# Optimization experiments

Hardware: AMD Instinct MI355X
Metric: run time of the kernel (lower is better)

## Reference

```python
import jax, jax.numpy as jnp
import numpy as np

D_MODEL = 768
N_HEADS = 12
N_KV = 4
D_HEAD = 64
WINDOW = 512
GLOBAL = 64
THETA = 10000.0


def setup_inputs() -> dict:
    key = jax.random.key(0)
    ks = jax.random.split(key, 5)
    B, T = 2, 2048
    s = D_MODEL ** -0.5
    return {
        "x": jax.random.normal(ks[0], (B, T, D_MODEL), jnp.float32),
        "wq": jax.random.normal(ks[1], (D_MODEL, N_HEADS * D_HEAD), jnp.float32) * s,
        "wk": jax.random.normal(ks[2], (D_MODEL, N_KV * D_HEAD), jnp.float32) * s,
        "wv": jax.random.normal(ks[3], (D_MODEL, N_KV * D_HEAD), jnp.float32) * s,
        "wo": jax.random.normal(ks[4], (N_HEADS * D_HEAD, D_MODEL), jnp.float32) * s,
    }


def _rotate_half(x):
    h = x.shape[-1] // 2
    return jnp.concatenate([-x[..., h:], x[..., :h]], axis=-1)


def _rope_tables(T, dtype):
    inv_freq = 1.0 / (THETA ** (jnp.arange(0, D_HEAD, 2, dtype=jnp.float32) / D_HEAD))
    freqs = jnp.outer(jnp.arange(T, dtype=jnp.float32), inv_freq)  # [T, D_HEAD/2]
    emb = jnp.concatenate([freqs, freqs], axis=-1)  # [T, D_HEAD]
    return jnp.cos(emb).astype(dtype), jnp.sin(emb).astype(dtype)


def reference(x, wq, wk, wv, wo):
    B, T, _ = x.shape
    # projections -> [B, H, T, D]
    q = (x @ wq).reshape(B, T, N_HEADS, D_HEAD).transpose(0, 2, 1, 3)
    k = (x @ wk).reshape(B, T, N_KV, D_HEAD).transpose(0, 2, 1, 3)
    v = (x @ wv).reshape(B, T, N_KV, D_HEAD).transpose(0, 2, 1, 3)
    # RoPE (broadcast [T,D] over batch/heads)
    cos, sin = _rope_tables(T, x.dtype)
    q = q * cos + _rotate_half(q) * sin
    k = k * cos + _rotate_half(k) * sin
    new_k, new_v = k, v  # kv cache before GQA expansion
    # GQA expansion: each kv head repeated kv_groups consecutive times
    groups = N_HEADS // N_KV
    k = jnp.repeat(k, groups, axis=1)
    v = jnp.repeat(v, groups, axis=1)
    scale = jnp.asarray(D_HEAD, x.dtype) ** 0.5
    scores = jnp.einsum("bhqd,bhkd->bhqk", q, k) / scale
    # sliding-window causal + global-token mask (Longformer-style)
    i = jnp.arange(T)[:, None]
    j = jnp.arange(T)[None, :]
    allowed = (j <= i) & ((j > i - WINDOW) | (j < GLOBAL) | (i < GLOBAL))
    scores = jnp.where(allowed, scores, -jnp.inf)
    weights = jax.nn.softmax(scores, axis=-1)
    out = jnp.einsum("bhqk,bhkd->bhqd", weights, v)
    out = out.transpose(0, 2, 1, 3).reshape(B, T, N_HEADS * D_HEAD)
    return out @ wo, (new_k, new_v)
```

## Files before the change

kernel.cpp:

```cpp
#include <hip/hip_runtime.h>
#include <hip/hip_bf16.h>

#define BATCH 2
#define SEQ 2048
#define DMODEL 768
#define NHEADS 12
#define NKV 4
#define DHEAD 64
#define WIN 512
#define GLB 64
#define ROWS (BATCH * SEQ)

typedef short short8 __attribute__((ext_vector_type(8)));
typedef float f32x4 __attribute__((ext_vector_type(4)));

__device__ inline short f2bs(float f) {
    unsigned u = __float_as_uint(f);
    return (short)((u + 0x7fffu + ((u >> 16) & 1u)) >> 16);
}

__device__ inline void cp16(const short* g, short* l) {
    __builtin_amdgcn_global_load_lds(
        (const __attribute__((address_space(1))) unsigned int*)g,
        (__attribute__((address_space(3))) unsigned int*)l, 16, 0, 0);
}

__global__ __launch_bounds__(256) void transp_all(
    const float* __restrict__ wq, const float* __restrict__ wk,
    const float* __restrict__ wv, const float* __restrict__ wo,
    short* __restrict__ wqkvT, short* __restrict__ woT,
    const float* __restrict__ x, short* __restrict__ xb) {
    __shared__ float t[32][33];
    int bid = blockIdx.x;
    if (bid >= 1536) {
        const long i = ((long)(bid - 1536) * 256 + threadIdx.x) * 8;
        float ff[8];
        *(float4*)&ff[0] = ((const float4*)(x + i))[0];
        *(float4*)&ff[4] = ((const float4*)(x + i))[1];
        short8 o;
#pragma unroll
        for (int j = 0; j < 8; ++j) o[j] = f2bs(ff[j]);
        *(short8*)(xb + i) = o;
        return;
    }
    const float* src; short* dst; int N;
    if (bid < 576)      { src = wq; dst = wqkvT; N = DMODEL; }
    else if (bid < 768) { src = wk; dst = wqkvT + DMODEL * DMODEL; N = 256; bid -= 576; }
    else if (bid < 960) { src = wv; dst = wqkvT + (DMODEL + 256) * DMODEL; N = 256; bid -= 768; }
    else                { src = wo; dst = woT; N = DMODEL; bid -= 960; }
    const int ntx = N >> 5;
    const int k0 = (bid / ntx) << 5, n0 = (bid % ntx) << 5;
    const int x_ = threadIdx.x & 31, y = threadIdx.x >> 5;
#pragma unroll
    for (int i = 0; i < 32; i += 8)
        t[y + i][x_] = src[(long)(k0 + y + i) * N + n0 + x_];
    __syncthreads();
#pragma unroll
    for (int i = 0; i < 32; i += 8)
        dst[(long)(n0 + y + i) * DMODEL + k0 + x_] = f2bs(t[x_][y + i]);
}

__global__ __launch_bounds__(256) void prep_kv(const float* __restrict__ Vin,
                                               short* __restrict__ Vout,
                                               float* Kc, short* __restrict__ Kb) {
    __shared__ float t[32][33];
    const int bid = blockIdx.x;
    if (bid < 2048) {
        const int tid = bid * 256 + threadIdx.x;
        const int j = tid & 31;
        const int kvh = (tid >> 5) & 3;
        const int row = tid >> 7;
        const int trow = row & (SEQ - 1), b = row >> 11;
        const float inv = expf(-(float)j * 0.2878231366f);
        float s, c;
        sincosf((float)trow * inv, &s, &c);
        const long off = ((long)(b * NKV + kvh) * SEQ + trow) << 6;
        float* p = Kc + off;
        const float x1 = p[j], x2 = p[j + 32];
        const float y1 = x1 * c - x2 * s, y2 = x2 * c + x1 * s;
        p[j] = y1;
        p[j + 32] = y2;
        Kb[off + j] = f2bs(y1);
        Kb[off + j + 32] = f2bs(y2);
    } else {
        const int b2 = bid - 2048;
        const int tx = b2 & 63, dy = (b2 >> 6) & 1;
        const long bkv = b2 >> 7;
        const float* ip = Vin + bkv * SEQ * DHEAD;
        short* op = Vout + bkv * DHEAD * SEQ;
        const int t0 = tx * 32, d0 = dy * 32;
        const int x = threadIdx.x & 31, y = threadIdx.x >> 5;
#pragma unroll
        for (int i = 0; i < 32; i += 8)
            t[y + i][x] = ip[(long)(t0 + y + i) * DHEAD + d0 + x];
        __syncthreads();
        const int pan = t0 >> 6, tin = t0 & 63;
#pragma unroll
        for (int i = 0; i < 32; i += 8)
            op[(long)pan * 4096 + (d0 + y + i) * 64 + tin + x] = f2bs(t[x][y + i]);
    }
}

template <int MODE>
__global__ __launch_bounds__(256) void gemm_tn(const short* __restrict__ A,
                                               const short* __restrict__ Bt,
                                               float* __restrict__ Cq,
                                               float* __restrict__ Ck,
                                               float* __restrict__ Cv,
                                               int M, int N, int K) {
    __shared__ short As_[2][128 * 64];
    __shared__ short Bs_[2][128 * 64];
    const int tid = threadIdx.x;
    const int lane = tid & 63, w = tid >> 6;
    const int m_ = lane & 15, quad = lane >> 4;
    const int sw = m_ & 7;
    const int wm = w >> 1, wn = w & 1;
    const long bm = (long)blockIdx.y * 128, bn = (long)blockIdx.x * 128;
    const int soff = (lane >> 3) * K + (((lane & 7) ^ (lane >> 3)) << 3);

    f32x4 acc[4][4];
#pragma unroll
    for (int i = 0; i < 4; ++i)
#pragma unroll
        for (int j = 0; j < 4; ++j) acc[i][j] = (f32x4){0.f, 0.f, 0.f, 0.f};

    auto stage = [&](int k0, int bs) {
#pragma unroll
        for (int r = 0; r < 8; ++r) {
            const int ch = (w << 3) + r;
            if (ch < 16)
                cp16(A + (bm + (ch << 3)) * K + k0 + soff, &As_[bs][ch << 9]);
            else
                cp16(Bt + (bn + ((ch - 16) << 3)) * K + k0 + soff,
                     &Bs_[bs][(ch - 16) << 9]);
        }
    };

    stage(0, 0);
    asm volatile("s_waitcnt vmcnt(0)" ::: "memory");
    asm volatile("s_barrier" ::: "memory");

    const int nk = K >> 6;
    for (int ks = 0; ks < nk; ++ks) {
        const int bs = ks & 1;
        if (ks + 1 < nk) stage((ks + 1) << 6, bs ^ 1);
#pragma unroll
        for (int kh = 0; kh < 2; ++kh) {
            short8 af[4], bf[4];
#pragma unroll
            for (int i = 0; i < 4; ++i)
                af[i] = *(const short8*)&As_[bs][(wm * 64 + i * 16 + m_) * 64 + (((kh * 4 + quad) ^ sw) << 3)];
#pragma unroll
            for (int j = 0; j < 4; ++j)
                bf[j] = *(const short8*)&Bs_[bs][(wn * 64 + j * 16 + m_) * 64 + (((kh * 4 + quad) ^ sw) << 3)];
            __builtin_amdgcn_s_setprio(1);
#pragma unroll
            for (int i = 0; i < 4; ++i)
#pragma unroll
                for (int j = 0; j < 4; ++j)
                    acc[i][j] = __builtin_amdgcn_mfma_f32_16x16x32_bf16(af[i], bf[j], acc[i][j], 0, 0, 0);
            __builtin_amdgcn_s_setprio(0);
        }
        if (ks + 1 < nk) {
            asm volatile("s_waitcnt vmcnt(0)" ::: "memory");
            asm volatile("s_barrier" ::: "memory");
        }
    }

#pragma unroll
    for (int i = 0; i < 4; ++i) {
        const int row0 = (int)bm + wm * 64 + i * 16 + quad * 4;
#pragma unroll
        for (int j = 0; j < 4; ++j) {
            const int col = (int)bn + wn * 64 + j * 16 + m_;
#pragma unroll
            for (int r = 0; r < 4; ++r) {
                const int rw = row0 + r;
                const float val = acc[i][j][r];
                if (MODE == 1) {
                    if (col < DMODEL) {
                        Cq[(long)rw * DMODEL + col] = val;
                    } else {
                        const int c2 = col - DMODEL;
                        const int hh = (c2 >> 6) & 3, d = c2 & 63;
                        long oidx = (((long)((rw >> 11) * NKV + hh) * SEQ + (rw & (SEQ - 1))) << 6) | d;
                        ((c2 >> 8) ? Cv : Ck)[oidx] = val;
                    }
                } else {
                    Cq[(long)rw * N + col] = val;
                }
            }
        }
    }
}

__global__ __launch_bounds__(384) void flash6(
    const float* __restrict__ Qf, const short* __restrict__ Kb,
    const short* __restrict__ Vt, short* __restrict__ ATT) {
    __shared__ short Kbuf[2][64 * 64];
    __shared__ short Vbuf[2][64 * 64];
    __shared__ short Pl[6][16 * 64];
    const int tid = threadIdx.x;
    const int w = tid >> 6, lane = tid & 63;
    const int m_ = lane & 15, quad = lane >> 4;
    const int sw = m_ & 7;
    const int bkv = blockIdx.x >> 6;
    const int t0 = (63 - (blockIdx.x & 63)) << 5;
    const int b = bkv >> 2, kvh = bkv & 3;
    const int h = kvh * 3 + (w >> 1);
    const int qg = w & 1;
    const int trw = t0 + (qg << 4);
    const int tq = trw + m_;
    const long kgb = ((long)bkv * SEQ) << 6;
    const long vgb = (long)bkv * SEQ * DHEAD;

    const int soff = ((lane >> 3) << 6) + (((lane & 7) ^ (lane >> 3)) << 3);

    short8 qf0, qf1;
    {
        const float* qpf = Qf + (long)(b * SEQ + tq) * DMODEL + h * DHEAD + quad * 8;
        float xx[8], yy[8];
        *(float4*)&xx[0] = ((const float4*)qpf)[0];
        *(float4*)&xx[4] = ((const float4*)qpf)[1];
        *(float4*)&yy[0] = ((const float4*)(qpf + 32))[0];
        *(float4*)&yy[4] = ((const float4*)(qpf + 32))[1];
#pragma unroll
        for (int jj = 0; jj < 8; ++jj) {
            const int j = quad * 8 + jj;
            const float inv = expf(-(float)j * 0.2878231366f);
            float s_, c_;
            sincosf((float)tq * inv, &s_, &c_);
            qf0[jj] = f2bs((xx[jj] * c_ - yy[jj] * s_) * 0.125f);
            qf1[jj] = f2bs((yy[jj] * c_ + xx[jj] * s_) * 0.125f);
        }
    }

    f32x4 of[4];
#pragma unroll
    for (int i = 0; i < 4; ++i) of[i] = (f32x4){0.f, 0.f, 0.f, 0.f};
    float mr = -1e30f, lr = 0.f;

    int wlo = t0 - (WIN - 1);
    if (wlo < GLB) wlo = GLB;
    wlo &= ~63;
    const int nwin = (t0 + 31 >= wlo) ? (((t0 + 31 - wlo) >> 6) + 1) : 0;
    const int ntile = 1 + nwin;
    auto kb_of = [&](int j) { return (j == 0) ? 0 : (wlo + ((j - 1) << 6)); };

    auto stage = [&](int kb, int bs) {
#pragma unroll
        for (int r = 0; r < 3; ++r) {
            const int ch = w + 6 * r;
            if (ch < 8) {
                cp16(Kb + kgb + ((long)(kb + (ch << 3)) << 6) + soff,
                     &Kbuf[bs][ch << 9]);
            } else if (ch < 16) {
                const int cv = ch - 8;
                cp16(Vt + vgb + (((long)kb >> 6) << 12) + (cv << 9) + soff,
                     &Vbuf[bs][cv << 9]);
            }
        }
    };

    stage(kb_of(0), 0);
    asm volatile("s_waitcnt vmcnt(0)" ::: "memory");
    asm volatile("s_barrier" ::: "memory");

    for (int tI = 0; tI < ntile; ++tI) {
        const int kb = kb_of(tI);
        const int bs = tI & 1;
        if (tI + 1 < ntile) stage(kb_of(tI + 1), bs ^ 1);

        short8 kf[8], vf[8];
#pragma unroll
        for (int st = 0; st < 4; ++st)
#pragma unroll
            for (int hh = 0; hh < 2; ++hh)
                kf[st * 2 + hh] = *(const short8*)&Kbuf[bs][(st * 16 + m_) * 64 + (((hh * 4 + quad) ^ sw) << 3)];
#pragma unroll
        for (int dt = 0; dt < 4; ++dt)
#pragma unroll
            for (int kh = 0; kh < 2; ++kh)
                vf[dt * 2 + kh] = *(const short8*)&Vbuf[bs][(dt * 16 + m_) * 64 + (((kh * 4 + quad) ^ sw) << 3)];

        f32x4 s[4];
        __builtin_amdgcn_s_setprio(1);
#pragma unroll
        for (int st = 0; st < 4; ++st) {
            f32x4 a = (f32x4){0.f, 0.f, 0.f, 0.f};
            a = __builtin_amdgcn_mfma_f32_16x16x32_bf16(kf[st * 2 + 0], qf0, a, 0, 0, 0);
            a = __builtin_amdgcn_mfma_f32_16x16x32_bf16(kf[st * 2 + 1], qf1, a, 0, 0, 0);
            s[st] = a;
        }
        __builtin_amdgcn_s_setprio(0);

        const bool fully = (kb + 63 <= trw) &&
                           ((kb >= trw + 16 - WIN) || (kb + 63 < GLB) || (trw + 15 < GLB));
        if (!fully) {
#pragma unroll
            for (int st = 0; st < 4; ++st) {
#pragma unroll
                for (int r = 0; r < 4; ++r) {
                    const int key = kb + st * 16 + quad * 4 + r;
                    const bool ok = (key <= tq) && ((key > tq - WIN) || (key < GLB) || (tq < GLB));
                    if (!ok) s[st][r] = -1e30f;
                }
            }
        }

        float tm = -1e30f;
#pragma unroll
        for (int st = 0; st < 4; ++st)
#pragma unroll
            for (int r = 0; r < 4; ++r) tm = fmaxf(tm, s[st][r]);
        tm = fmaxf(tm, __shfl_xor(tm, 16, 64));
        tm = fmaxf(tm, __shfl_xor(tm, 32, 64));
        if (!__all(tm <= mr)) {
            const float mnew = fmaxf(mr, tm);
            const float alpha = __expf(mr - mnew);
            mr = mnew;
            lr *= alpha;
#pragma unroll
            for (int dt = 0; dt < 4; ++dt)
#pragma unroll
                for (int r = 0; r < 4; ++r) of[dt][r] *= alpha;
        }
        float rs = 0.f;
#pragma unroll
        for (int st = 0; st < 4; ++st) {
            float p0 = __expf(s[st][0] - mr);
            float p1 = __expf(s[st][1] - mr);
            float p2 = __expf(s[st][2] - mr);
            float p3 = __expf(s[st][3] - mr);
            rs += (p0 + p1) + (p2 + p3);
            union { short sh[4]; unsigned long long u; } pk;
            pk.sh[0] = f2bs(p0); pk.sh[1] = f2bs(p1);
            pk.sh[2] = f2bs(p2); pk.sh[3] = f2bs(p3);
            *(unsigned long long*)&Pl[w][m_ * 64 + (((st * 2 + (quad >> 1)) ^ sw) << 3) + ((quad & 1) << 2)] = pk.u;
        }
        rs += __shfl_xor(rs, 16, 64);
        rs += __shfl_xor(rs, 32, 64);
        lr += rs;

        short8 pf[2];
#pragma unroll
        for (int kh = 0; kh < 2; ++kh)
            pf[kh] = *(const short8*)&Pl[w][m_ * 64 + (((kh * 4 + quad) ^ sw) << 3)];

        __builtin_amdgcn_s_setprio(1);
#pragma unroll
        for (int dt = 0; dt < 4; ++dt) {
            of[dt] = __builtin_amdgcn_mfma_f32_16x16x32_bf16(vf[dt * 2 + 0], pf[0], of[dt], 0, 0, 0);
            of[dt] = __builtin_amdgcn_mfma_f32_16x16x32_bf16(vf[dt * 2 + 1], pf[1], of[dt], 0, 0, 0);
        }
        __builtin_amdgcn_s_setprio(0);

        if (tI + 1 < ntile) {
            asm volatile("s_waitcnt vmcnt(0)" ::: "memory");
            asm volatile("s_barrier" ::: "memory");
        }
    }

    const float inv = 1.0f / lr;
    short* op = ATT + (long)(b * SEQ + tq) * DMODEL + h * DHEAD + quad * 4;
#pragma unroll
    for (int dt = 0; dt < 4; ++dt) {
        union { short sh[4]; unsigned long long u; } pk;
#pragma unroll
        for (int r = 0; r < 4; ++r) pk.sh[r] = f2bs(of[dt][r] * inv);
        *(unsigned long long*)(op + dt * 16) = pk.u;
    }
}

extern "C" void kernel_launch(void* const* d_in, const int* in_sizes, int n_in,
                              void* d_out, int out_size, void* d_ws, size_t ws_size,
                              hipStream_t stream) {
    const float* x = (const float*)d_in[0];
    const float* wq = (const float*)d_in[1];
    const float* wk = (const float*)d_in[2];
    const float* wv = (const float*)d_in[3];
    const float* wo = (const float*)d_in[4];
    float* out = (float*)d_out;
    float* out_k = out + (long)ROWS * DMODEL;
    float* out_v = out_k + (long)BATCH * NKV * SEQ * DHEAD;

    short* regA = (short*)d_ws;
    short* wqkvT = regA;
    short* ATTb = regA;
    short* woT = regA + (long)ROWS * DMODEL;
    short* KbB = woT + (long)DMODEL * DMODEL;
    short* VtB = KbB + (long)BATCH * NKV * SEQ * DHEAD;
    short* xb = VtB + (long)BATCH * NKV * SEQ * DHEAD;

    transp_all<<<3072, 256, 0, stream>>>(wq, wk, wv, wo, wqkvT, woT, x, xb);
    gemm_tn<1><<<dim3((DMODEL + 2 * NKV * DHEAD) / 128, ROWS / 128), 256, 0, stream>>>(
        xb, wqkvT, out, out_k, out_v, ROWS, DMODEL + 2 * NKV * DHEAD, DMODEL);
    prep_kv<<<2048 + 1024, 256, 0, stream>>>(out_v, VtB, out_k, KbB);
    flash6<<<BATCH * NKV * (SEQ / 32), 384, 0, stream>>>(out, KbB, VtB, ATTb);
    gemm_tn<0><<<dim3(DMODEL / 128, ROWS / 128), 256, 0, stream>>>(
        ATTb, woT, out, nullptr, nullptr, ROWS, DMODEL, DMODEL);
}
```

Measured before the change: 138.3 us.

## Fuse K RoPE and V transpose into QKV GEMM epilogue, use 64-row tiles

Removes the separate prep_kv kernel. The QKV GEMM epilogue now applies RoPE to K, writes both fp32 and bf16 K, and writes V in fp32 plus a transposed bf16 panel layout. To make the RoPE pairing local to one wave, and to raise block count, the GEMM tile height drops from 128 to 64 rows for both GEMMs. This saves one launch and a full read and write pass over K and V, but the epilogue now does sincos work and scattered stores, and the smaller tiles reuse data less.

```diff
diff --git a/kernel.cpp b/kernel.cpp
--- a/kernel.cpp
+++ b/kernel.cpp
@@ -60,79 +60,36 @@
         dst[(long)(n0 + y + i) * DMODEL + k0 + x_] = f2bs(t[x_][y + i]);
 }
 
-__global__ __launch_bounds__(256) void prep_kv(const float* __restrict__ Vin,
-                                               short* __restrict__ Vout,
-                                               float* Kc, short* __restrict__ Kb) {
-    __shared__ float t[32][33];
-    const int bid = blockIdx.x;
-    if (bid < 2048) {
-        const int tid = bid * 256 + threadIdx.x;
-        const int j = tid & 31;
-        const int kvh = (tid >> 5) & 3;
-        const int row = tid >> 7;
-        const int trow = row & (SEQ - 1), b = row >> 11;
-        const float inv = expf(-(float)j * 0.2878231366f);
-        float s, c;
-        sincosf((float)trow * inv, &s, &c);
-        const long off = ((long)(b * NKV + kvh) * SEQ + trow) << 6;
-        float* p = Kc + off;
-        const float x1 = p[j], x2 = p[j + 32];
-        const float y1 = x1 * c - x2 * s, y2 = x2 * c + x1 * s;
-        p[j] = y1;
-        p[j + 32] = y2;
-        Kb[off + j] = f2bs(y1);
-        Kb[off + j + 32] = f2bs(y2);
-    } else {
-        const int b2 = bid - 2048;
-        const int tx = b2 & 63, dy = (b2 >> 6) & 1;
-        const long bkv = b2 >> 7;
-        const float* ip = Vin + bkv * SEQ * DHEAD;
-        short* op = Vout + bkv * DHEAD * SEQ;
-        const int t0 = tx * 32, d0 = dy * 32;
-        const int x = threadIdx.x & 31, y = threadIdx.x >> 5;
-#pragma unroll
-        for (int i = 0; i < 32; i += 8)
-            t[y + i][x] = ip[(long)(t0 + y + i) * DHEAD + d0 + x];
-        __syncthreads();
-        const int pan = t0 >> 6, tin = t0 & 63;
-#pragma unroll
-        for (int i = 0; i < 32; i += 8)
-            op[(long)pan * 4096 + (d0 + y + i) * 64 + tin + x] = f2bs(t[x][y + i]);
-    }
-}
-
 template <int MODE>
-__global__ __launch_bounds__(256) void gemm_tn(const short* __restrict__ A,
-                                               const short* __restrict__ Bt,
-                                               float* __restrict__ Cq,
-                                               float* __restrict__ Ck,
-                                               float* __restrict__ Cv,
-                                               int M, int N, int K) {
-    __shared__ short As_[2][128 * 64];
+__global__ __launch_bounds__(256) void gemm_tn(
+    const short* __restrict__ A, const short* __restrict__ Bt,
+    float* __restrict__ Cq, float* __restrict__ Ck, float* __restrict__ Cv,
+    short* __restrict__ Kb, short* __restrict__ Vt, int M, int N, int K) {
+    __shared__ short As_[2][64 * 64];
     __shared__ short Bs_[2][128 * 64];
     const int tid = threadIdx.x;
     const int lane = tid & 63, w = tid >> 6;
     const int m_ = lane & 15, quad = lane >> 4;
     const int sw = m_ & 7;
     const int wm = w >> 1, wn = w & 1;
-    const long bm = (long)blockIdx.y * 128, bn = (long)blockIdx.x * 128;
+    const long bm = (long)blockIdx.y * 64, bn = (long)blockIdx.x * 128;
     const int soff = (lane >> 3) * K + (((lane & 7) ^ (lane >> 3)) << 3);
 
-    f32x4 acc[4][4];
-#pragma unroll
-    for (int i = 0; i < 4; ++i)
+    f32x4 acc[2][4];
+#pragma unroll
+    for (int i = 0; i < 2; ++i)
 #pragma unroll
         for (int j = 0; j < 4; ++j) acc[i][j] = (f32x4){0.f, 0.f, 0.f, 0.f};
 
     auto stage = [&](int k0, int bs) {
 #pragma unroll
-        for (int r = 0; r < 8; ++r) {
-            const int ch = (w << 3) + r;
-            if (ch < 16)
+        for (int r = 0; r < 6; ++r) {
+            const int ch = w * 6 + r;
+            if (ch < 8)
                 cp16(A + (bm + (ch << 3)) * K + k0 + soff, &As_[bs][ch << 9]);
             else
-                cp16(Bt + (bn + ((ch - 16) << 3)) * K + k0 + soff,
-                     &Bs_[bs][(ch - 16) << 9]);
+                cp16(Bt + (bn + ((ch - 8) << 3)) * K + k0 + soff,
+                     &Bs_[bs][(ch - 8) << 9]);
         }
     };
 
@@ -146,16 +103,16 @@
         if (ks + 1 < nk) stage((ks + 1) << 6, bs ^ 1);
 #pragma unroll
         for (int kh = 0; kh < 2; ++kh) {
-            short8 af[4], bf[4];
-#pragma unroll
-            for (int i = 0; i < 4; ++i)
-                af[i] = *(const short8*)&As_[bs][(wm * 64 + i * 16 + m_) * 64 + (((kh * 4 + quad) ^ sw) << 3)];
+            short8 af[2], bf[4];
+#pragma unroll
+            for (int i = 0; i < 2; ++i)
+                af[i] = *(const short8*)&As_[bs][(wm * 32 + i * 16 + m_) * 64 + (((kh * 4 + quad) ^ sw) << 3)];
 #pragma unroll
             for (int j = 0; j < 4; ++j)
                 bf[j] = *(const short8*)&Bs_[bs][(wn * 64 + j * 16 + m_) * 64 + (((kh * 4 + quad) ^ sw) << 3)];
             __builtin_amdgcn_s_setprio(1);
 #pragma unroll
-            for (int i = 0; i < 4; ++i)
+            for (int i = 0; i < 2; ++i)
 #pragma unroll
                 for (int j = 0; j < 4; ++j)
                     acc[i][j] = __builtin_amdgcn_mfma_f32_16x16x32_bf16(af[i], bf[j], acc[i][j], 0, 0, 0);
@@ -167,28 +124,65 @@
         }
     }
 
-#pragma unroll
-    for (int i = 0; i < 4; ++i) {
-        const int row0 = (int)bm + wm * 64 + i * 16 + quad * 4;
-#pragma unroll
-        for (int j = 0; j < 4; ++j) {
-            const int col = (int)bn + wn * 64 + j * 16 + m_;
-#pragma unroll
-            for (int r = 0; r < 4; ++r) {
-                const int rw = row0 + r;
-                const float val = acc[i][j][r];
-                if (MODE == 1) {
-                    if (col < DMODEL) {
-                        Cq[(long)rw * DMODEL + col] = val;
-                    } else {
-                        const int c2 = col - DMODEL;
-                        const int hh = (c2 >> 6) & 3, d = c2 & 63;
-                        long oidx = (((long)((rw >> 11) * NKV + hh) * SEQ + (rw & (SEQ - 1))) << 6) | d;
-                        ((c2 >> 8) ? Cv : Ck)[oidx] = val;
-                    }
-                } else {
-                    Cq[(long)rw * N + col] = val;
+    if (MODE == 0 || bn < DMODEL) {
+        const int stride = (MODE == 1) ? DMODEL : N;
+#pragma unroll
+        for (int i = 0; i < 2; ++i) {
+            const int row0 = (int)bm + wm * 32 + i * 16 + quad * 4;
+#pragma unroll
+            for (int j = 0; j < 4; ++j) {
+                const int col = (int)bn + wn * 64 + j * 16 + m_;
+#pragma unroll
+                for (int r = 0; r < 4; ++r)
+                    Cq[(long)(row0 + r) * stride + col] = acc[i][j][r];
+            }
+        }
+    } else if (bn < DMODEL + 256) {
+        const int kvh = ((int)(bn - DMODEL) >> 6) + wn;
+#pragma unroll
+        for (int i = 0; i < 2; ++i) {
+            const int row0 = (int)bm + wm * 32 + i * 16 + quad * 4;
+            const int t = row0 & (SEQ - 1), b = row0 >> 11;
+            const long base0 = ((long)(b * NKV + kvh) * SEQ) << 6;
+#pragma unroll
+            for (int j = 0; j < 2; ++j) {
+                const int d = j * 16 + m_;
+                const float invf = expf(-(float)d * 0.2878231366f);
+#pragma unroll
+                for (int r = 0; r < 4; ++r) {
+                    const int tt = t + r;
+                    float s_, c_;
+                    sincosf((float)tt * invf, &s_, &c_);
+                    const float x1 = acc[i][j][r], x2 = acc[i][j + 2][r];
+                    const float y1 = x1 * c_ - x2 * s_;
+                    const float y2 = x2 * c_ + x1 * s_;
+                    const long o = base0 + ((long)tt << 6) + d;
+                    Ck[o] = y1;
+                    Ck[o + 32] = y2;
+                    Kb[o] = f2bs(y1);
+                    Kb[o + 32] = f2bs(y2);
                 }
+            }
+        }
+    } else {
+        const int kvh = ((int)(bn - (DMODEL + 256)) >> 6) + wn;
+#pragma unroll
+        for (int i = 0; i < 2; ++i) {
+            const int row0 = (int)bm + wm * 32 + i * 16 + quad * 4;
+            const int t = row0 & (SEQ - 1), b = row0 >> 11;
+            const long bkvi = (long)(b * NKV + kvh);
+            const long vtbase = (bkvi << 17) + ((long)(t >> 6) << 12) + (t & 63);
+#pragma unroll
+            for (int j = 0; j < 4; ++j) {
+                const int d = j * 16 + m_;
+                union { short sh[4]; unsigned long long u; } pk;
+#pragma unroll
+                for (int r = 0; r < 4; ++r) {
+                    const float v = acc[i][j][r];
+                    Cv[((bkvi * SEQ + t + r) << 6) + d] = v;
+                    pk.sh[r] = f2bs(v);
+                }
+                *(unsigned long long*)&Vt[vtbase + ((long)d << 6)] = pk.u;
             }
         }
     }
@@ -393,10 +387,9 @@
     short* xb = VtB + (long)BATCH * NKV * SEQ * DHEAD;
 
     transp_all<<<3072, 256, 0, stream>>>(wq, wk, wv, wo, wqkvT, woT, x, xb);
-    gemm_tn<1><<<dim3((DMODEL + 2 * NKV * DHEAD) / 128, ROWS / 128), 256, 0, stream>>>(
-        xb, wqkvT, out, out_k, out_v, ROWS, DMODEL + 2 * NKV * DHEAD, DMODEL);
-    prep_kv<<<2048 + 1024, 256, 0, stream>>>(out_v, VtB, out_k, KbB);
+    gemm_tn<1><<<dim3((DMODEL + 2 * NKV * DHEAD) / 128, ROWS / 64), 256, 0, stream>>>(
+        xb, wqkvT, out, out_k, out_v, KbB, VtB, ROWS, DMODEL + 2 * NKV * DHEAD, DMODEL);
     flash6<<<BATCH * NKV * (SEQ / 32), 384, 0, stream>>>(out, KbB, VtB, ATTb);
-    gemm_tn<0><<<dim3(DMODEL / 128, ROWS / 128), 256, 0, stream>>>(
-        ATTb, woT, out, nullptr, nullptr, ROWS, DMODEL, DMODEL);
-}
+    gemm_tn<0><<<dim3(DMODEL / 128, ROWS / 64), 256, 0, stream>>>(
+        ATTb, woT, out, nullptr, nullptr, nullptr, nullptr, ROWS, DMODEL, DMODEL);
+}
```

Measured after the change: 134.7 us, median of 2. -2.6%, faster.
